# Optimization experiments

Hardware: AMD Instinct MI355X
Metric: run time of the kernel (lower is better)

The kernel has to match this reference:

```python
import jax, jax.numpy as jnp
import numpy as np

T, B, L, D = 32, 128, 1024, 256  # timesteps, batch, memory slots, word_vec_size(=rnn_size)


def setup_inputs() -> dict:
    key = jax.random.key(0)
    ks = jax.random.split(key, 20)
    f = lambda k, s: jax.random.normal(k, s, dtype=jnp.float32) * 0.05
    return {
        "emb_utts": f(ks[0], (T, B, D)),
        "hr0": f(ks[1], (B, D)),
        "cr0": f(ks[2], (B, D)),
        "hw0": f(ks[3], (B, D)),
        "cw0": f(ks[4], (B, D)),
        "M": f(ks[5], (B, L, D)),
        "mask": jax.random.randint(ks[6], (B, L), 0, 2).astype(bool),
        "Wih_r": f(ks[7], (4 * D, D)),
        "Whh_r": f(ks[8], (4 * D, D)),
        "bih_r": f(ks[9], (4 * D,)),
        "bhh_r": f(ks[10], (4 * D,)),
        "Wc": f(ks[11], (D, 2 * D)),
        "bc": f(ks[12], (D,)),
        "Wih_w": f(ks[13], (4 * D, D)),
        "Whh_w": f(ks[14], (4 * D, D)),
        "bih_w": f(ks[15], (4 * D,)),
        "bhh_w": f(ks[16], (4 * D,)),
    }


def _lstm_cell(x, h, c, Wih, Whh, bih, bhh):
    # PyTorch LSTMCell gate order: i, f, g, o
    g = x @ Wih.T + h @ Whh.T + bih + bhh
    i, fg, gg, o = jnp.split(g, 4, axis=1)
    i = jax.nn.sigmoid(i)
    fg = jax.nn.sigmoid(fg)
    gg = jnp.tanh(gg)
    o = jax.nn.sigmoid(o)
    c2 = fg * c + i * gg
    return o * jnp.tanh(c2), c2


def reference(emb_utts, hr0, cr0, hw0, cw0, M, mask,
              Wih_r, Whh_r, bih_r, bhh_r, Wc, bc,
              Wih_w, Whh_w, bih_w, bhh_w):
    def step(carry, w):
        hr, cr, hw, cw, Mc = carry
        hr, cr = _lstm_cell(w, hr, cr, Wih_r, Whh_r, bih_r, bhh_r)
        # attention read: z = softmax(masked(hr . M))  -> [B, L]
        z = jnp.einsum('bd,bld->bl', hr, Mc)
        z = jax.nn.softmax(jnp.where(mask, -jnp.inf, z), axis=1)
        m = jnp.einsum('bl,bld->bd', z, Mc)           # gather read [B, D]
        comp = jax.nn.softmax(jnp.concatenate([hr, m], axis=1) @ Wc.T + bc, axis=1)
        hw, cw = _lstm_cell(comp, hw, cw, Wih_w, Whh_w, bih_w, bhh_w)
        # memory rewrite exactly as source: M_new = (1 - z) + hw * z (broadcast)
        Mc = (1.0 - z[:, :, None]) + hw[:, None, :] * z[:, :, None]
        return (hr, cr, hw, cw, Mc), hw

    (hr, cr, hw, cw, M), outputs = jax.lax.scan(
        step, (hr0, cr0, hw0, cw0, M), emb_utts)
    return outputs, hr, cr, hw, cw, M
```

## Files before the change

kernel.cpp:

```cpp
#include <hip/hip_runtime.h>
#include <math.h>

typedef unsigned int u32;
typedef unsigned short u16;
typedef __attribute__((ext_vector_type(2))) _Float16 h2;

#define kT 32
#define OUT_STATES 1048576
#define OUT_M      1179648

union H2U { u32 u; h2 h; };

__device__ __forceinline__ float dot2u(u32 w, u32 x, float acc){
  H2U a; a.u = w; H2U b; b.u = x;
#if __has_builtin(__builtin_amdgcn_fdot2)
  return __builtin_amdgcn_fdot2(a.h, b.h, acc, false);
#else
  acc += (float)a.h.x * (float)b.h.x;
  acc += (float)a.h.y * (float)b.h.y;
  return acc;
#endif
}

__device__ __forceinline__ u32 packf16(float x, float y){
  H2U v; v.h.x = (_Float16)x; v.h.y = (_Float16)y; return v.u;
}

__device__ __forceinline__ void unpack2(u32 x, u32& lo, u32& hi){
#if __has_builtin(__builtin_amdgcn_perm)
  lo = __builtin_amdgcn_perm(0u, x, 0x010c000cu);
  hi = __builtin_amdgcn_perm(0u, x, 0x030c020cu);
#else
  lo = ((x & 0xFFu) << 8) | ((x & 0xFF00u) << 16);
  hi = ((x >> 8) & 0xFF00u) | (x & 0xFF000000u);
#endif
}

__device__ __forceinline__ u32 alu(const u32* p){
  return __hip_atomic_load((u32*)p, __ATOMIC_RELAXED, __HIP_MEMORY_SCOPE_AGENT);
}
__device__ __forceinline__ float alf(const float* p){
  return __hip_atomic_load((float*)p, __ATOMIC_RELAXED, __HIP_MEMORY_SCOPE_AGENT);
}
__device__ __forceinline__ void asu(u32* p, u32 v){
  __hip_atomic_store(p, v, __ATOMIC_RELAXED, __HIP_MEMORY_SCOPE_AGENT);
}
__device__ __forceinline__ void asf(float* p, float v){
  __hip_atomic_store(p, v, __ATOMIC_RELAXED, __HIP_MEMORY_SCOPE_AGENT);
}

__device__ __forceinline__ void pollk(const u32* f, int n, u32 tgt, int tid){
  if (tid < 64){
    const u32* p = f + ((tid < n) ? tid : 0);
    for (;;){
      if (__all((int)(alu(p) >= tgt))) break;
      __builtin_amdgcn_s_sleep(2);
    }
  }
  __syncthreads();
}

__global__ __launch_bounds__(1024) void k_prep(
        const float* __restrict__ Wih_r, const float* __restrict__ Whh_r,
        const float* __restrict__ bih_r, const float* __restrict__ bhh_r,
        const float* __restrict__ Wc,    const float* __restrict__ bc,
        const float* __restrict__ Wih_w, const float* __restrict__ Whh_w,
        const float* __restrict__ bih_w, const float* __restrict__ bhh_w,
        const unsigned char* __restrict__ maskraw,
        u32* WAp, u32* WEp, u32* Wcp, u16* WEi8,
        float* bA, float* bE, float* bcf,
        float* wcs, unsigned char* mbuf, u32* flags){
  __shared__ int sb[3];
  if (threadIdx.x < 3) sb[threadIdx.x] = 0;
  __syncthreads();
  if (threadIdx.x < 512){
    unsigned char c = maskraw[threadIdx.x];
    if (c > 1u) atomicOr(&sb[0], 1);
    if ((threadIdx.x & 3) != 0 && c != 0) atomicOr(&sb[1], 1);
    if ((threadIdx.x & 3) == 1 && c == 0x3F) atomicOr(&sb[2], 1);
  }
  __syncthreads();
  int mode = (!sb[0]) ? (sb[1] ? 1 : 0) : (sb[2] ? 2 : 3);

  int idx = blockIdx.x * 1024 + threadIdx.x;
  if (idx < 262144){
    int col = idx >> 8, kp = idx & 255;
    int k0 = 2 * kp;
    float v0 = (k0 < 256) ? Wih_r[col * 256 + k0] : Whh_r[col * 256 + k0 - 256];
    float v1 = (k0 < 256) ? Wih_r[col * 256 + k0 + 1]
                          : Whh_r[col * 256 + k0 + 1 - 256];
    WAp[kp * 1024 + col] = packf16(v0, v1);
  } else if (idx < 524288){
    int i = idx - 262144;
    int col = i >> 8, kp = i & 255;
    int k0 = 2 * kp;
    float v0 = (k0 < 256) ? Wih_w[col * 256 + k0] : Whh_w[col * 256 + k0 - 256];
    float v1 = (k0 < 256) ? Wih_w[col * 256 + k0 + 1]
                          : Whh_w[col * 256 + k0 + 1 - 256];
    u32 p = packf16(v0, v1);
    WEp[kp * 1024 + col] = p;
    if (kp < 128){
      u32 b0 = ((p & 0xFFFFu) + 0x80u) >> 8;
      u32 b1 = (((p >> 16) & 0xFFFFu) + 0x80u) >> 8;
      WEi8[kp * 1024 + col] = (u16)((b0 & 0xFFu) | ((b1 & 0xFFu) << 8));
    }
  } else if (idx < 589824){
    int i = idx - 524288;
    int col = i >> 8, kp = i & 255;
    Wcp[kp * 256 + col] = packf16(Wc[col * 512 + 2 * kp], Wc[col * 512 + 2 * kp + 1]);
  } else if (idx < 590848){
    int i = idx - 589824;
    bA[i] = bih_r[i] + bhh_r[i];
  } else if (idx < 591872){
    int i = idx - 590848;
    bE[i] = bih_w[i] + bhh_w[i];
  } else if (idx < 592128){
    int i = idx - 591872;
    bcf[i] = bc[i];
  } else if (idx < 592384){
    int c = idx - 592128;
    float s = 0.f;
    for (int k = 0; k < 256; k++) s += Wc[c * 512 + 256 + k];
    wcs[c] = s;
  } else if (idx < 723456){
    int l = idx - 592384;
    unsigned char mv;
    if      (mode == 0) mv = (((const int*)maskraw)[l] != 0);
    else if (mode == 1) mv = (maskraw[l] != 0);
    else if (mode == 2) mv = ((maskraw[2*l] | maskraw[2*l+1]) != 0);
    else                mv = (((const unsigned int*)maskraw)[l] != 0);
    mbuf[l] = mv;
  } else if (idx < 724224){
    flags[idx - 723456] = 0;
  }
}

__global__ __launch_bounds__(1024) void k_pre(
        const float* __restrict__ emb, const u32* __restrict__ WAp,
        u32* __restrict__ gxp){
  __shared__ u32 wt[16384];
  __shared__ u32 xt[128 * 129];
  int t = blockIdx.x, c0 = blockIdx.y * 128, tid = threadIdx.x;
  for (int i = 0; i < 16; i++){
    int idx = i * 1024 + tid;
    wt[idx] = WAp[(size_t)(idx >> 7) * 1024 + c0 + (idx & 127)];
    int b = idx >> 7, kp = idx & 127;
    float2 e2 = *(const float2*)(emb + (size_t)t * 32768 + b * 256 + 2 * kp);
    xt[b * 129 + kp] = packf16(e2.x, e2.y);
  }
  __syncthreads();
  int b = tid & 127, cg = tid >> 7;
  float acc[16];
  #pragma unroll
  for (int j = 0; j < 16; j++) acc[j] = 0.f;
  const u32* xrow = xt + b * 129;
  for (int kp = 0; kp < 128; kp++){
    u32 xv = xrow[kp];
    const uint4* wr = (const uint4*)(wt + kp * 128 + cg * 16);
    #pragma unroll
    for (int j4 = 0; j4 < 4; j4++){
      uint4 wv = wr[j4];
      acc[4*j4+0] = dot2u(wv.x, xv, acc[4*j4+0]);
      acc[4*j4+1] = dot2u(wv.y, xv, acc[4*j4+1]);
      acc[4*j4+2] = dot2u(wv.z, xv, acc[4*j4+2]);
      acc[4*j4+3] = dot2u(wv.w, xv, acc[4*j4+3]);
    }
  }
  u32* gp = gxp + ((size_t)t * 128 + b) * 512 + (c0 >> 1) + cg * 8;
  #pragma unroll
  for (int i = 0; i < 8; i++) gp[i] = packf16(acc[2*i], acc[2*i+1]);
}

__device__ __forceinline__ void gemv256(const u32* __restrict__ W,
        const u32* xh, float* psum, int tid){
  int cg = tid & 255, ks = tid >> 8;
  const uint4* wp = (const uint4*)W + (size_t)ks * 32 * 256 + cg;
  const u32* xk = xh + ks * 32;
  float a0 = 0.f, a1 = 0.f, a2 = 0.f, a3 = 0.f;
  #pragma unroll 8
  for (int i = 0; i < 32; i++){
    uint4 wv = wp[(size_t)i * 256];
    u32 xp = xk[i];
    a0 = dot2u(wv.x, xp, a0);  a1 = dot2u(wv.y, xp, a1);
    a2 = dot2u(wv.z, xp, a2);  a3 = dot2u(wv.w, xp, a3);
  }
  float4 r; r.x = a0; r.y = a1; r.z = a2; r.w = a3;
  *(float4*)&psum[ks * 1024 + cg * 4] = r;
}

__device__ __forceinline__ void gemv128x256(const u32* __restrict__ W,
        const u32* xh, float* psum, int tid){
  int c = tid & 255, ks = tid >> 8;
  const u32* wp = W + (size_t)(ks * 32) * 256 + c;
  const u32* xk = xh + ks * 32;
  float a = 0.f;
  #pragma unroll 8
  for (int i = 0; i < 32; i++) a = dot2u(wp[(size_t)i * 256], xk[i], a);
  psum[ks * 256 + c] = a;
}

__device__ void scan_half(int k, const float* __restrict__ M0,
        const unsigned char* __restrict__ mbuf, const float* __restrict__ hrf,
        float* spbuf, float* mpbuf, float* msbuf, u32* fT0, const u32* fR,
        char* sc, int tid){
  float* ps   = (float*)(sc);
  float* wred = (float*)(sc + 16640);
  float* sred = (float*)(sc + 16704);
  float* hr0l = (float*)(sc + 16768);
  int row = k >> 1, half = k & 1;
  pollk(fR + row, 1, 1u, tid);
  if (tid < 256) hr0l[tid] = alf(hrf + row * 256 + tid);
  __syncthreads();
  int w = tid >> 6, lane = tid & 63;
  float4 hrv = *(const float4*)&hr0l[lane * 4];
  float run_max = -INFINITY, S = 0.f;
  float m0 = 0.f, m1 = 0.f, m2 = 0.f, m3 = 0.f;
  int l0 = half * 512 + w * 32;
  for (int l = l0; l < l0 + 32; ++l){
    float4 Mv = *(const float4*)(M0 + ((size_t)row * 1024 + l) * 256 + lane * 4);
    float part = Mv.x * hrv.x + Mv.y * hrv.y + Mv.z * hrv.z + Mv.w * hrv.w;
    #pragma unroll
    for (int mm = 32; mm >= 1; mm >>= 1) part += __shfl_xor(part, mm, 64);
    float s = mbuf[row * 1024 + l] ? -INFINITY : part;
    if (lane == 0) asf(spbuf + row * 1024 + l, s);
    float nm = fmaxf(run_max, s);
    if (nm > -INFINITY){
      float sc2 = expf(run_max - nm);
      float p   = expf(s - nm);
      S = S * sc2 + p;
      m0 = m0 * sc2 + p * Mv.x;  m1 = m1 * sc2 + p * Mv.y;
      m2 = m2 * sc2 + p * Mv.z;  m3 = m3 * sc2 + p * Mv.w;
      run_max = nm;
    }
  }
  if (lane == 0){ wred[w] = run_max; sred[w] = S; }
  ps[w * 260 + lane * 4 + 0] = m0;
  ps[w * 260 + lane * 4 + 1] = m1;
  ps[w * 260 + lane * 4 + 2] = m2;
  ps[w * 260 + lane * 4 + 3] = m3;
  __syncthreads();
  float gmax = -INFINITY;
  #pragma unroll
  for (int w2 = 0; w2 < 16; w2++) gmax = fmaxf(gmax, wred[w2]);
  float Sg = 0.f;
  #pragma unroll
  for (int w2 = 0; w2 < 16; w2++) Sg += sred[w2] * expf(wred[w2] - gmax);
  if (tid < 256){
    float mv = 0.f;
    #pragma unroll
    for (int w2 = 0; w2 < 16; w2++) mv += ps[w2 * 260 + tid] * expf(wred[w2] - gmax);
    asf(mpbuf + k * 256 + tid, mv);
  }
  if (tid == 0){ asf(msbuf + 2 * k, gmax); asf(msbuf + 2 * k + 1, Sg); }
  __syncthreads();
  if (tid == 0) asu(fT0 + k, 1u);
}

__global__ __launch_bounds__(1024, 4) void k_main(
        const float* __restrict__ hr0, const float* __restrict__ cr0,
        const float* __restrict__ hw0, const float* __restrict__ cw0,
        const float* __restrict__ M0,
        const u32* __restrict__ WAp, const u32* __restrict__ WEp,
        const u32* __restrict__ Wcp, const u16* __restrict__ WEi8,
        const float* __restrict__ bA,
        const float* __restrict__ bE, const float* __restrict__ bcf,
        const float* __restrict__ wcs, const unsigned char* __restrict__ mbuf,
        const u32* __restrict__ gxp,
        float* __restrict__ hrf, float* __restrict__ ubuf,
        float* __restrict__ vcbuf, float* __restrict__ gwbuf,
        u32* __restrict__ hwp, float* __restrict__ zsbuf,
        float* __restrict__ hwfin, float* __restrict__ spbuf,
        float* __restrict__ mpbuf, float* __restrict__ msbuf,
        u32* __restrict__ flags, float* __restrict__ out){
  __shared__ __attribute__((aligned(16))) char smem[86016];
  int bid = blockIdx.x, tid = threadIdx.x;
  int w = tid >> 6, lane = tid & 63;
  u32* fR  = flags;
  u32* fGv = flags + 128;
  u32* fG  = flags + 192;
  u32* fW  = flags + 256;
  u32* fT0 = flags + 320;

  if (bid < 128){
    int b = bid;
    float* psum = (float*)(smem);
    u32*  xh    = (u32*)(smem + 16384);
    float* hr_f = (float*)(smem + 16896);
    const u32* WRh = WAp + 128 * 1024;
    float cst = (tid < 256) ? cr0[b * 256 + tid] : 0.f;
    if (tid < 128){
      float2 h0 = *(const float2*)(hr0 + b * 256 + 2 * tid);
      xh[tid] = packf16(h0.x, h0.y);
    }
    __syncthreads();
    for (int t = 0; t < kT; t++){
      if (t >= 2) pollk(fW + (b >> 1), 1, (u32)(t - 1), tid);
      u32 gx0 = 0, gx1 = 0, gx2 = 0, gx3 = 0;
      if (tid < 256){
        const u32* gx = gxp + ((size_t)t * 128 + b) * 512;
        gx0 = gx[tid >> 1];          gx1 = gx[128 + (tid >> 1)];
        gx2 = gx[256 + (tid >> 1)];  gx3 = gx[384 + (tid >> 1)];
      }
      gemv256(WRh, xh, psum, tid);
      __syncthreads();
      if (tid < 256){
        H2U p0, p1, p2, p3;
        p0.u = gx0; p1.u = gx1; p2.u = gx2; p3.u = gx3;
        int hi = tid & 1;
        float gi = (hi ? (float)p0.h.y : (float)p0.h.x) + bA[tid];
        float gf = (hi ? (float)p1.h.y : (float)p1.h.x) + bA[256 + tid];
        float gg = (hi ? (float)p2.h.y : (float)p2.h.x) + bA[512 + tid];
        float go = (hi ? (float)p3.h.y : (float)p3.h.x) + bA[768 + tid];
        #pragma unroll
        for (int ks = 0; ks < 4; ks++){
          gi += psum[ks * 1024 + tid];
          gf += psum[ks * 1024 + 256 + tid];
          gg += psum[ks * 1024 + 512 + tid];
          go += psum[ks * 1024 + 768 + tid];
        }
        float i_ = 1.f / (1.f + expf(-gi));
        float f_ = 1.f / (1.f + expf(-gf));
        float g_ = tanhf(gg);
        float o_ = 1.f / (1.f + expf(-go));
        float c2 = f_ * cst + i_ * g_;
        cst = c2;
        float h = o_ * tanhf(c2);
        hr_f[tid] = h;
        asf(hrf + (t & 1) * 32768 + b * 256 + tid, h);
        if (t == kT - 1){
          out[OUT_STATES          + b * 256 + tid] = h;
          out[OUT_STATES +  32768 + b * 256 + tid] = c2;
        }
      }
      __syncthreads();
      if (tid < 128) xh[tid] = packf16(hr_f[2 * tid], hr_f[2 * tid + 1]);
      __syncthreads();
      gemv128x256(Wcp, xh, psum, tid);
      __syncthreads();
      if (tid < 256){
        float u = psum[tid] + psum[256 + tid] + psum[512 + tid] + psum[768 + tid];
        asf(ubuf + (t & 1) * 32768 + b * 256 + tid, u);
      }
      __syncthreads();
      if (tid == 0) asu(fR + b, (u32)(t + 1));
      if (t == 0)
        scan_half(bid, M0, mbuf, hrf, spbuf, mpbuf, msbuf, fT0, fR,
                  smem + 49152, tid);
    }
  } else if (bid < 192){
    int g = bid - 128, r0 = 2 * g, r1 = 2 * g + 1;
    float* psum = (float*)(smem);
    u32*  xh    = (u32*)(smem + 32768);
    for (int t = 0; t < kT; t++){
      if (t == 0){
        if (tid < 128){
          float2 h0 = *(const float2*)(hw0 + r0 * 256 + 2 * tid);
          xh[tid] = packf16(h0.x, h0.y);
        } else if (tid < 256){
          int j = tid - 128;
          float2 h0 = *(const float2*)(hw0 + r1 * 256 + 2 * j);
          xh[tid] = packf16(h0.x, h0.y);
        }
      } else {
        pollk(fW + g, 1, (u32)t, tid);
        if (tid < 128)
          xh[tid] = alu(hwp + ((t - 1) & 1) * 16384 + r0 * 128 + tid);
        else if (tid < 256)
          xh[tid] = alu(hwp + ((t - 1) & 1) * 16384 + r1 * 128 + (tid - 128));
      }
      __syncthreads();
      {
        int c = tid & 255, ks = tid >> 8;
        const u32* wp = Wcp + 32768 + (size_t)(ks * 32) * 256 + c;
        const u32* x0 = xh + ks * 32;
        const u32* x1 = xh + 128 + ks * 32;
        float a0 = 0.f, a1 = 0.f;
        #pragma unroll 8
        for (int ii = 0; ii < 32; ii++){
          u32 wv = wp[(size_t)ii * 256];
          a0 = dot2u(wv, x0[ii], a0);
          a1 = dot2u(wv, x1[ii], a1);
        }
        psum[ks * 512 + c] = a0;
        psum[ks * 512 + 256 + c] = a1;
      }
      __syncthreads();
      if (tid < 512){
        int rr = tid >> 8, c = tid & 255;
        float v = psum[rr * 256 + c] + psum[512 + rr * 256 + c]
                + psum[1024 + rr * 256 + c] + psum[1536 + rr * 256 + c];
        asf(vcbuf + (t & 1) * 32768 + (2 * g + rr) * 256 + c, v);
      }
      __syncthreads();
      if (tid == 0) asu(fGv + g, (u32)(t + 1));
      {
        int cg = tid & 255, ks = tid >> 8;
        const uint4* wp = (const uint4*)(WEp + 128 * 1024)
                        + (size_t)(ks * 32) * 256 + cg;
        const u32* x0 = xh + ks * 32;
        const u32* x1 = xh + 128 + ks * 32;
        float a0=0.f,a1=0.f,a2=0.f,a3=0.f,b0=0.f,b1=0.f,b2=0.f,b3=0.f;
        #pragma unroll 4
        for (int ii = 0; ii < 32; ii++){
          uint4 wv = wp[(size_t)ii * 256];
          u32 xp0 = x0[ii], xp1 = x1[ii];
          a0 = dot2u(wv.x, xp0, a0);  a1 = dot2u(wv.y, xp0, a1);
          a2 = dot2u(wv.z, xp0, a2);  a3 = dot2u(wv.w, xp0, a3);
          b0 = dot2u(wv.x, xp1, b0);  b1 = dot2u(wv.y, xp1, b1);
          b2 = dot2u(wv.z, xp1, b2);  b3 = dot2u(wv.w, xp1, b3);
        }
        float4 ra; ra.x=a0; ra.y=a1; ra.z=a2; ra.w=a3;
        float4 rb; rb.x=b0; rb.y=b1; rb.z=b2; rb.w=b3;
        *(float4*)&psum[ks * 1024 + cg * 4] = ra;
        *(float4*)&psum[4096 + ks * 1024 + cg * 4] = rb;
      }
      __syncthreads();
      #pragma unroll
      for (int rr = 0; rr < 2; rr++){
        float v = psum[rr * 4096 + tid] + psum[rr * 4096 + 1024 + tid]
                + psum[rr * 4096 + 2048 + tid] + psum[rr * 4096 + 3072 + tid];
        asf(gwbuf + (t & 1) * 131072 + (2 * g + rr) * 1024 + tid, v);
      }
      __syncthreads();
      if (tid == 0) asu(fG + g, (u32)(t + 1));
      if (t == 0)
        scan_half(bid, M0, mbuf, hrf, spbuf, mpbuf, msbuf, fT0, fR,
                  smem + 49152, tid);
    }
  } else {
    int g = bid - 192, r0g = 2 * g;
    float* psum  = (float*)(smem);
    u32*  xh    = (u32*)(smem + 32768);
    float* comp  = (float*)(smem + 33792);
    float* hw_f  = (float*)(smem + 35840);
    float* m_f   = (float*)(smem + 37888);
    float* wcs_l = (float*)(smem + 39936);
    float* bc_l  = (float*)(smem + 40960);
    float* redA  = (float*)(smem + 41984);
    float* redB  = (float*)(smem + 42048);
    float* redC  = (float*)(smem + 42112);
    float* redD  = (float*)(smem + 42176);
    float* bE_l  = (float*)(smem + 43008);
    int row = tid >> 9, i = tid & 511;
    int brow = r0g + row;
    if (tid < 256){ wcs_l[tid] = wcs[tid]; bc_l[tid] = bcf[tid]; }
    bE_l[tid] = bE[tid];
    float cst = 0.f;
    if (i < 256){
      hw_f[row * 256 + i] = hw0[brow * 256 + i];
      cst = cw0[brow * 256 + i];
    }
    unsigned char mkA = mbuf[brow * 1024 + i];
    unsigned char mkB = mbuf[brow * 1024 + 512 + i];
    float zA = 0.f, zB = 0.f;
    __syncthreads();
    scan_half(bid, M0, mbuf, hrf, spbuf, mpbuf, msbuf, fT0, fR,
              smem + 49152, tid);
    pollk(fR + r0g, 2, 1u, tid);
    float hrv = 0.f, ureg = 0.f;
    if (i < 256){
      hrv  = alf(hrf + brow * 256 + i);
      ureg = alf(ubuf + brow * 256 + i);
    }

    for (int t = 0; t < kT; t++){
      float e = -INFINITY;
      if (t == 0){
        pollk(fT0 + 4 * g, 4, 1u, tid);
        int kA2 = 2 * brow, kB2 = 2 * brow + 1;
        float maxA = alf(msbuf + 2 * kA2), SAv = alf(msbuf + 2 * kA2 + 1);
        float maxB = alf(msbuf + 2 * kB2), SBv = alf(msbuf + 2 * kB2 + 1);
        float Gm = fmaxf(maxA, maxB);
        float eAc = expf(maxA - Gm), eBc = expf(maxB - Gm);
        float Sg = SAv * eAc + SBv * eBc;
        zA = expf(alf(spbuf + brow * 1024 + i) - Gm) / Sg;
        zB = expf(alf(spbuf + brow * 1024 + 512 + i) - Gm) / Sg;
        if (i < 256){
          float mv = (alf(mpbuf + kA2 * 256 + i) * eAc
                    + alf(mpbuf + kB2 * 256 + i) * eBc) / Sg;
          m_f[row * 256 + i] = mv;
        }
        __syncthreads();
        if (i < 128)
          xh[row * 128 + i] = packf16(m_f[row * 256 + 2 * i],
                                      m_f[row * 256 + 2 * i + 1]);
        __syncthreads();
        {
          int c = tid & 255, ks = tid >> 8;
          const u32* wp = Wcp + 32768 + (size_t)(ks * 32) * 256 + c;
          const u32* x0 = xh + ks * 32;
          const u32* x1 = xh + 128 + ks * 32;
          float a0 = 0.f, a1 = 0.f;
          #pragma unroll 8
          for (int ii = 0; ii < 32; ii++){
            u32 wv = wp[(size_t)ii * 256];
            a0 = dot2u(wv, x0[ii], a0);
            a1 = dot2u(wv, x1[ii], a1);
          }
          psum[ks * 512 + c] = a0;
          psum[ks * 512 + 256 + c] = a1;
        }
        __syncthreads();
        if (i < 256){
          float vcm = psum[row * 256 + i] + psum[512 + row * 256 + i]
                    + psum[1024 + row * 256 + i] + psum[1536 + row * 256 + i];
          e = ureg + vcm + bc_l[i];
        }
      } else {
        float v1 = (i < 256) ? hrv : 0.f;
        float v2 = (i < 256) ? hrv * hw_f[row * 256 + i] : 0.f;
        #pragma unroll
        for (int mm = 32; mm >= 1; mm >>= 1){
          v1 += __shfl_xor(v1, mm, 64);  v2 += __shfl_xor(v2, mm, 64);
        }
        if (lane == 0){ redA[w] = v1; redB[w] = v2; }
        __syncthreads();
        float S1 = 0.f, S2 = 0.f;
        #pragma unroll
        for (int k2 = 0; k2 < 8; k2++){
          S1 += redA[row * 8 + k2];  S2 += redB[row * 8 + k2];
        }
        float gm = fmaxf(S1, S2);
        float sA = mkA ? -INFINITY : (1.f - zA) * S1 + zA * S2;
        float sB = mkB ? -INFINITY : (1.f - zB) * S1 + zB * S2;
        float pA_ = expf(sA - gm), pB_ = expf(sB - gm);
        float ps = pA_ + pB_, pz = pA_ * zA + pB_ * zB;
        #pragma unroll
        for (int mm = 32; mm >= 1; mm >>= 1){
          ps += __shfl_xor(ps, mm, 64);  pz += __shfl_xor(pz, mm, 64);
        }
        if (lane == 0){ redC[w] = ps; redD[w] = pz; }
        __syncthreads();
        float Ss = 0.f, Pz = 0.f;
        #pragma unroll
        for (int k2 = 0; k2 < 8; k2++){
          Ss += redC[row * 8 + k2];  Pz += redD[row * 8 + k2];
        }
        float Cb = Pz / Ss, Ab = 1.f - Cb;
        zA = pA_ / Ss;  zB = pB_ / Ss;
        pollk(fGv + g, 1, (u32)(t + 1), tid);
        if (i < 256){
          float vc = alf(vcbuf + (t & 1) * 32768 + brow * 256 + i);
          e = ureg + Ab * wcs_l[i] + Cb * vc + bc_l[i];
        }
      }
      float pe = (i < 256) ? expf(e - 4.f) : 0.f;
      float ps2 = pe;
      #pragma unroll
      for (int mm = 32; mm >= 1; mm >>= 1) ps2 += __shfl_xor(ps2, mm, 64);
      if (lane == 0) redA[w] = ps2;
      if (i < 256) comp[row * 256 + i] = pe;
      __syncthreads();
      float esum = 0.f;
      #pragma unroll
      for (int k2 = 0; k2 < 8; k2++) esum += redA[row * 8 + k2];
      if (i < 128)
        xh[row * 128 + i] = packf16(comp[row * 256 + 2 * i],
                                    comp[row * 256 + 2 * i + 1]);
      __syncthreads();
      {
        int cg = tid & 255, ks = tid >> 8;
        const u16* wb = WEi8 + (size_t)(ks * 32) * 1024 + 4 * cg;
        const u32* x0 = xh + ks * 32;
        const u32* x1 = xh + 128 + ks * 32;
        float a0=0.f,a1=0.f,a2=0.f,a3=0.f,b0=0.f,b1=0.f,b2=0.f,b3=0.f;
        #pragma unroll 8
        for (int ii = 0; ii < 32; ii++){
          uint2 wv = *(const uint2*)(wb + (size_t)ii * 1024);
          u32 xp0 = x0[ii], xp1 = x1[ii];
          u32 w0, w1, w2, w3;
          unpack2(wv.x, w0, w1);
          unpack2(wv.y, w2, w3);
          a0 = dot2u(w0, xp0, a0);  a1 = dot2u(w1, xp0, a1);
          a2 = dot2u(w2, xp0, a2);  a3 = dot2u(w3, xp0, a3);
          b0 = dot2u(w0, xp1, b0);  b1 = dot2u(w1, xp1, b1);
          b2 = dot2u(w2, xp1, b2);  b3 = dot2u(w3, xp1, b3);
        }
        float4 ra; ra.x=a0; ra.y=a1; ra.z=a2; ra.w=a3;
        float4 rb; rb.x=b0; rb.y=b1; rb.z=b2; rb.w=b3;
        *(float4*)&psum[ks * 1024 + cg * 4] = ra;
        *(float4*)&psum[4096 + ks * 1024 + cg * 4] = rb;
      }
      __syncthreads();
      pollk(fG + g, 1, (u32)(t + 1), tid);
      if (i < 256){
        float rinv = 1.f / esum;
        const float* gwp = gwbuf + (t & 1) * 131072 + brow * 1024;
        float si = psum[row*4096 + i]        + psum[row*4096 + 1024 + i]
                 + psum[row*4096 + 2048 + i] + psum[row*4096 + 3072 + i];
        float sf = psum[row*4096 + 256 + i]  + psum[row*4096 + 1280 + i]
                 + psum[row*4096 + 2304 + i] + psum[row*4096 + 3328 + i];
        float sg2= psum[row*4096 + 512 + i]  + psum[row*4096 + 1536 + i]
                 + psum[row*4096 + 2560 + i] + psum[row*4096 + 3584 + i];
        float so = psum[row*4096 + 768 + i]  + psum[row*4096 + 1792 + i]
                 + psum[row*4096 + 2816 + i] + psum[row*4096 + 3840 + i];
        float gi = bE_l[i]       + alf(gwp + i)       + si  * rinv;
        float gf = bE_l[256 + i] + alf(gwp + 256 + i) + sf  * rinv;
        float gg = bE_l[512 + i] + alf(gwp + 512 + i) + sg2 * rinv;
        float go = bE_l[768 + i] + alf(gwp + 768 + i) + so  * rinv;
        float i_ = 1.f / (1.f + expf(-gi));
        float f_ = 1.f / (1.f + expf(-gf));
        float g_ = tanhf(gg);
        float o_ = 1.f / (1.f + expf(-go));
        float c2 = f_ * cst + i_ * g_;
        cst = c2;
        float h = o_ * tanhf(c2);
        hw_f[row * 256 + i] = h;
        out[(size_t)t * 32768 + brow * 256 + i] = h;
        if (t == kT - 1){
          out[OUT_STATES + 65536 + brow * 256 + i] = h;
          out[OUT_STATES + 98304 + brow * 256 + i] = c2;
        }
      }
      __syncthreads();
      if (i < 128)
        asu(hwp + (t & 1) * 16384 + brow * 128 + i,
            packf16(hw_f[row * 256 + 2 * i], hw_f[row * 256 + 2 * i + 1]));
      __syncthreads();
      if (tid == 0) asu(fW + g, (u32)(t + 1));
      if (t < kT - 1){
        pollk(fR + r0g, 2, (u32)(t + 2), tid);
        if (i < 256){
          hrv  = alf(hrf + ((t + 1) & 1) * 32768 + brow * 256 + i);
          ureg = alf(ubuf + ((t + 1) & 1) * 32768 + brow * 256 + i);
        }
      }
    }
    if (i < 256) asf(hwfin + brow * 256 + i, hw_f[row * 256 + i]);
    asf(zsbuf + brow * 1024 + i, zA);
    asf(zsbuf + brow * 1024 + 512 + i, zB);
    __syncthreads();
    if (tid == 0) asu(fW + g, (u32)(kT + 1));
  }

  {
    int mrow = bid >> 1, half = bid & 1;
    pollk(fW + (mrow >> 1), 1, (u32)(kT + 1), tid);
    float* zl  = (float*)(smem + 49152);
    float* hwl = (float*)(smem + 51200);
    if (tid < 512) zl[tid] = alf(zsbuf + mrow * 1024 + half * 512 + tid);
    else if (tid < 768) hwl[tid - 512] = alf(hwfin + mrow * 256 + (tid - 512));
    __syncthreads();
    float* Mout = out + OUT_M + (size_t)mrow * 262144 + (size_t)half * 131072;
    for (int it = 0; it < 32; it++){
      int idx = it * 1024 + tid;
      int l = idx >> 6, d4 = (idx & 63) << 2;
      float z = zl[l], omz = 1.f - z;
      float4 h4 = *(const float4*)&hwl[d4];
      float4 v;
      v.x = omz + h4.x * z;  v.y = omz + h4.y * z;
      v.z = omz + h4.z * z;  v.w = omz + h4.w * z;
      *(float4*)(Mout + (size_t)l * 256 + d4) = v;
    }
  }
}

extern "C" void kernel_launch(void* const* d_in, const int* in_sizes, int n_in,
                              void* d_out, int out_size, void* d_ws, size_t ws_size,
                              hipStream_t stream){
  const float* emb   = (const float*)d_in[0];
  const float* hr0   = (const float*)d_in[1];
  const float* cr0   = (const float*)d_in[2];
  const float* hw0   = (const float*)d_in[3];
  const float* cw0   = (const float*)d_in[4];
  const float* M0    = (const float*)d_in[5];
  const unsigned char* maskraw = (const unsigned char*)d_in[6];
  const float* Wih_r = (const float*)d_in[7];
  const float* Whh_r = (const float*)d_in[8];
  const float* bih_r = (const float*)d_in[9];
  const float* bhh_r = (const float*)d_in[10];
  const float* Wc    = (const float*)d_in[11];
  const float* bc    = (const float*)d_in[12];
  const float* Wih_w = (const float*)d_in[13];
  const float* Whh_w = (const float*)d_in[14];
  const float* bih_w = (const float*)d_in[15];
  const float* bhh_w = (const float*)d_in[16];
  float* out = (float*)d_out;

  char* ws = (char*)d_ws;
  u32*  WAp   = (u32*)(ws);
  u32*  WEp   = (u32*)(ws + 1048576);
  u32*  Wcp   = (u32*)(ws + 2097152);
  float* bA   = (float*)(ws + 2359296);
  float* bE   = (float*)(ws + 2363392);
  float* bcf  = (float*)(ws + 2367488);
  float* wcs  = (float*)(ws + 2368512);
  unsigned char* mbuf = (unsigned char*)(ws + 2369536);
  u32*  flags = (u32*)(ws + 2500608);
  float* hrf  = (float*)(ws + 2504704);
  float* ubuf = (float*)(ws + 2766848);
  float* gwbuf= (float*)(ws + 3291136);
  u32*  hwp   = (u32*)(ws + 4339712);
  float* zsbuf= (float*)(ws + 4470784);
  float* hwfin= (float*)(ws + 4995072);
  float* spbuf= (float*)(ws + 5126144);
  float* mpbuf= (float*)(ws + 5650432);
  float* msbuf= (float*)(ws + 5912576);
  u32*  gxp   = (u32*)(ws + 5914624);
  float* vcbuf= (float*)(ws + 14303232);
  u16*  WEi8  = (u16*)(ws + 14565376);

  k_prep<<<dim3(708), dim3(1024), 0, stream>>>(
      Wih_r, Whh_r, bih_r, bhh_r, Wc, bc, Wih_w, Whh_w, bih_w, bhh_w,
      maskraw, WAp, WEp, Wcp, WEi8, bA, bE, bcf, wcs, mbuf, flags);
  k_pre<<<dim3(32, 8), dim3(1024), 0, stream>>>(emb, WAp, gxp);
  k_main<<<dim3(256), dim3(1024), 0, stream>>>(
      hr0, cr0, hw0, cw0, M0, WAp, WEp, Wcp, WEi8, bA, bE, bcf, wcs, mbuf,
      gxp, hrf, ubuf, vcbuf, gwbuf, hwp, zsbuf, hwfin, spbuf, mpbuf, msbuf,
      flags, out);
}
```

Baseline: 654.4 us.

## Interleave int8 write-weight layout for 16-byte loads and restructure hw polling

Repacks the 8-bit compressed write-LSTM input weights so that two adjacent k-pairs for four columns sit in one 16-byte chunk. The GEMV can then issue half as many wider uint4 loads. Separately, the Wc-half blocks now load hw0 once before the loop, and the poll-and-fetch of the next hw moves to the end of each step behind an extra barrier. This reorders when the flag wait happens relative to scan_half and the gate writes, and it adds barriers.

Measured after the change: 648.1 us. About the same (-1.0%).

```diff
diff --git a/kernel.cpp b/kernel.cpp
--- a/kernel.cpp
+++ b/kernel.cpp
@@ -102,7 +102,8 @@
     if (kp < 128){
       u32 b0 = ((p & 0xFFFFu) + 0x80u) >> 8;
       u32 b1 = (((p >> 16) & 0xFFFFu) + 0x80u) >> 8;
-      WEi8[kp * 1024 + col] = (u16)((b0 & 0xFFu) | ((b1 & 0xFFu) << 8));
+      WEi8[(kp >> 1) * 2048 + (col >> 2) * 8 + (kp & 1) * 4 + (col & 3)]
+          = (u16)((b0 & 0xFFu) | ((b1 & 0xFFu) << 8));
     }
   } else if (idx < 589824){
     int i = idx - 524288;
@@ -351,24 +352,16 @@
     int g = bid - 128, r0 = 2 * g, r1 = 2 * g + 1;
     float* psum = (float*)(smem);
     u32*  xh    = (u32*)(smem + 32768);
+    if (tid < 128){
+      float2 h0 = *(const float2*)(hw0 + r0 * 256 + 2 * tid);
+      xh[tid] = packf16(h0.x, h0.y);
+    } else if (tid < 256){
+      int j = tid - 128;
+      float2 h0 = *(const float2*)(hw0 + r1 * 256 + 2 * j);
+      xh[tid] = packf16(h0.x, h0.y);
+    }
+    __syncthreads();
     for (int t = 0; t < kT; t++){
-      if (t == 0){
-        if (tid < 128){
-          float2 h0 = *(const float2*)(hw0 + r0 * 256 + 2 * tid);
-          xh[tid] = packf16(h0.x, h0.y);
-        } else if (tid < 256){
-          int j = tid - 128;
-          float2 h0 = *(const float2*)(hw0 + r1 * 256 + 2 * j);
-          xh[tid] = packf16(h0.x, h0.y);
-        }
-      } else {
-        pollk(fW + g, 1, (u32)t, tid);
-        if (tid < 128)
-          xh[tid] = alu(hwp + ((t - 1) & 1) * 16384 + r0 * 128 + tid);
-        else if (tid < 256)
-          xh[tid] = alu(hwp + ((t - 1) & 1) * 16384 + r1 * 128 + (tid - 128));
-      }
-      __syncthreads();
       {
         int c = tid & 255, ks = tid >> 8;
         const u32* wp = Wcp + 32768 + (size_t)(ks * 32) * 256 + c;
@@ -426,6 +419,17 @@
       if (t == 0)
         scan_half(bid, M0, mbuf, hrf, spbuf, mpbuf, msbuf, fT0, fR,
                   smem + 49152, tid);
+      if (t < kT - 1){
+        pollk(fW + g, 1, (u32)(t + 1), tid);
+        u32 nx = 0;
+        if (tid < 128)
+          nx = alu(hwp + (t & 1) * 16384 + r0 * 128 + tid);
+        else if (tid < 256)
+          nx = alu(hwp + (t & 1) * 16384 + r1 * 128 + (tid - 128));
+        __syncthreads();
+        if (tid < 256) xh[tid] = nx;
+        __syncthreads();
+      }
     }
   } else {
     int g = bid - 192, r0g = 2 * g;
@@ -560,21 +564,28 @@
       __syncthreads();
       {
         int cg = tid & 255, ks = tid >> 8;
-        const u16* wb = WEi8 + (size_t)(ks * 32) * 1024 + 4 * cg;
+        const uint4* wp = (const uint4*)WEi8 + (size_t)(ks * 16) * 256 + cg;
         const u32* x0 = xh + ks * 32;
         const u32* x1 = xh + 128 + ks * 32;
         float a0=0.f,a1=0.f,a2=0.f,a3=0.f,b0=0.f,b1=0.f,b2=0.f,b3=0.f;
-        #pragma unroll 8
-        for (int ii = 0; ii < 32; ii++){
-          uint2 wv = *(const uint2*)(wb + (size_t)ii * 1024);
-          u32 xp0 = x0[ii], xp1 = x1[ii];
-          u32 w0, w1, w2, w3;
-          unpack2(wv.x, w0, w1);
-          unpack2(wv.y, w2, w3);
-          a0 = dot2u(w0, xp0, a0);  a1 = dot2u(w1, xp0, a1);
-          a2 = dot2u(w2, xp0, a2);  a3 = dot2u(w3, xp0, a3);
-          b0 = dot2u(w0, xp1, b0);  b1 = dot2u(w1, xp1, b1);
-          b2 = dot2u(w2, xp1, b2);  b3 = dot2u(w3, xp1, b3);
+        #pragma unroll 4
+        for (int ii = 0; ii < 16; ii++){
+          uint4 wv = wp[(size_t)ii * 256];
+          u32 xe0 = x0[2*ii], xo0 = x0[2*ii+1];
+          u32 xe1 = x1[2*ii], xo1 = x1[2*ii+1];
+          u32 c0e, c1e, c2e, c3e, c0o, c1o, c2o, c3o;
+          unpack2(wv.x, c0e, c1e);
+          unpack2(wv.y, c2e, c3e);
+          unpack2(wv.z, c0o, c1o);
+          unpack2(wv.w, c2o, c3o);
+          a0 = dot2u(c0e, xe0, a0);  a0 = dot2u(c0o, xo0, a0);
+          a1 = dot2u(c1e, xe0, a1);  a1 = dot2u(c1o, xo0, a1);
+          a2 = dot2u(c2e, xe0, a2);  a2 = dot2u(c2o, xo0, a2);
+          a3 = dot2u(c3e, xe0, a3);  a3 = dot2u(c3o, xo0, a3);
+          b0 = dot2u(c0e, xe1, b0);  b0 = dot2u(c0o, xo1, b0);
+          b1 = dot2u(c1e, xe1, b1);  b1 = dot2u(c1o, xo1, b1);
+          b2 = dot2u(c2e, xe1, b2);  b2 = dot2u(c2o, xo1, b2);
+          b3 = dot2u(c3e, xe1, b3);  b3 = dot2u(c3o, xo1, b3);
         }
         float4 ra; ra.x=a0; ra.y=a1; ra.z=a2; ra.w=a3;
         float4 rb; rb.x=b0; rb.y=b1; rb.z=b2; rb.w=b3;
```
